# Kernel optimization log

Measured on AMD Instinct MI355X. Metric: run time of the kernel, lower is better.

The kernel has to match this reference:

```python
import jax, jax.numpy as jnp
import numpy as np

IOU_THRESHOLD = 0.5


def setup_inputs() -> dict:
    key = jax.random.key(0)
    k1, k2, k3 = jax.random.split(key, 3)
    B, N = 4, 8192
    # valid boxes: top-left in [0,200), width/height in [1,51)
    xy = jax.random.uniform(k1, (B, N, 2), dtype=jnp.float32) * 200.0
    wh = jax.random.uniform(k2, (B, N, 2), dtype=jnp.float32) * 50.0 + 1.0
    boxes = jnp.concatenate([xy, xy + wh], axis=-1)  # [B,N,4] (x1,y1,x2,y2)
    scores = jax.random.uniform(k3, (B, N), dtype=jnp.float32)
    return {"boxes": boxes, "scores": scores}


def _soft_nms_single(boxes, scores):
    # boxes: [N,4], scores: [N]
    x1, y1, x2, y2 = boxes[:, 0], boxes[:, 1], boxes[:, 2], boxes[:, 3]
    inter_w = jnp.maximum(0.0, jnp.minimum(x2[:, None], x2[None, :]) - jnp.maximum(x1[:, None], x1[None, :]))
    inter_h = jnp.maximum(0.0, jnp.minimum(y2[:, None], y2[None, :]) - jnp.maximum(y1[:, None], y1[None, :]))
    inter = inter_w * inter_h  # [N,N]
    area = (x2 - x1) * (y2 - y1)  # [N]
    union = area[:, None] + area[None, :] - inter
    iou = inter / union  # [N,N]
    weight = jnp.exp(-iou / IOU_THRESHOLD)  # [N,N]
    adjusted = weight @ scores  # [N] : adjusted_scores[i] = sum_j w[i,j]*s[j]
    w = jax.nn.softmax(adjusted, axis=0)  # [N]
    return w @ boxes  # [4]


def reference(boxes, scores):
    return jax.vmap(_soft_nms_single)(boxes, scores)  # [B,4]
```

## Files before the change

kernel.cpp:

```cpp
#include <hip/hip_runtime.h>
#include <hip/hip_bf16.h>
#include <type_traits>

#define BATCH   4
#define NBOX    8192
#define BLOCK   256
#define TSZ     256
#define NT      (NBOX / TSZ)
#define NPAIRS  (NT * (NT + 1) / 2)
#define NBINS   2048
#define SUBS    8
#define SUBSZ   (NBOX / SUBS)
#define STH     512

__device__ __forceinline__ float bf2f(unsigned short u) {
    union { unsigned int i; float f; } c;
    c.i = ((unsigned int)u) << 16;
    return c.f;
}

__device__ __forceinline__ bool box_plausible(float x1, float y1, float x2, float y2) {
    bool ok = (x1 == x1) && (y1 == y1) && (x2 == x2) && (y2 == y2);
    ok = ok && fabsf(x1) < 1e4f && fabsf(y1) < 1e4f && fabsf(x2) < 1e4f && fabsf(y2) < 1e4f;
    ok = ok && x1 >= -1.0f && x1 <= 300.0f && y1 >= -1.0f && y1 <= 300.0f;
    const float w = x2 - x1, h = y2 - y1;
    ok = ok && w >= -0.1f && w <= 80.0f && h >= -0.1f && h <= 80.0f;
    return ok;
}

__device__ __forceinline__ bool wave_probe_is_f32(const void* boxes_raw) {
    const int lane = threadIdx.x & 63;
    const float* bf = (const float*)boxes_raw;
    const bool okf = box_plausible(bf[lane * 4 + 0], bf[lane * 4 + 1],
                                   bf[lane * 4 + 2], bf[lane * 4 + 3]);
    const unsigned short* bh = (const unsigned short*)boxes_raw;
    const bool okh = box_plausible(bf2f(bh[lane * 4 + 0]), bf2f(bh[lane * 4 + 1]),
                                   bf2f(bh[lane * 4 + 2]), bf2f(bh[lane * 4 + 3]));
    const unsigned long long mf = __ballot(okf);
    const unsigned long long mh = __ballot(okh);
    return __popcll(mf) >= __popcll(mh);
}

__device__ __forceinline__ float4 load_box(const void* boxes_raw, size_t idx, bool isf32) {
    if (isf32) {
        return reinterpret_cast<const float4*>(boxes_raw)[idx];
    } else {
        const ushort4 u = reinterpret_cast<const ushort4*>(boxes_raw)[idx];
        return make_float4(bf2f(u.x), bf2f(u.y), bf2f(u.z), bf2f(u.w));
    }
}

__device__ __forceinline__ float load_score(const void* scores_raw, size_t idx, bool isf32) {
    return isf32 ? ((const float*)scores_raw)[idx]
                 : bf2f(((const unsigned short*)scores_raw)[idx]);
}

__device__ __forceinline__ int key_bin(float v) {
    const int bb = (int)(v * 8.0f);
    return min(NBINS - 1, max(0, bb));
}

#define CEXP (-2.8853900817779268f)

__device__ __forceinline__ float pair_weight(
    float ix1, float iy1, float ix2, float iy2, float iarea,
    const float4& bj, float jarea)
{
    float w = fminf(ix2, bj.z) - fmaxf(ix1, bj.x);
    float h = fminf(iy2, bj.w) - fmaxf(iy1, bj.y);
    w = fmaxf(w, 0.0f);
    h = fmaxf(h, 0.0f);
    const float inter = w * h;
    const float uni   = iarea + jarea - inter;
    const float arg   = (CEXP * inter) * __builtin_amdgcn_rcpf(uni);
    return __builtin_amdgcn_exp2f(arg);
}

__global__ __launch_bounds__(STH) void sort_kernel(
    const void* __restrict__ boxes_raw, const void* __restrict__ scores_raw,
    float4* __restrict__ sboxes, float* __restrict__ sscores,
    float* __restrict__ adj,
    float* __restrict__ minx1c, float* __restrict__ maxx2c,
    int* __restrict__ pairlist, int* __restrict__ count)
{
    __shared__ int hist[NBINS];
    __shared__ int bmin[NBINS];
    __shared__ int hist2[NBINS];
    __shared__ int wsum[STH / 64];
    __shared__ float sminT[NT], smaxT[NT];
    __shared__ int scnt;

    const int b    = blockIdx.x / SUBS;
    const int sub  = blockIdx.x % SUBS;
    const int tid  = threadIdx.x;
    const int lane = tid & 63;
    const int wv   = tid >> 6;
    const bool isf32 = wave_probe_is_f32(boxes_raw);
    const size_t base = (size_t)b * NBOX;

#pragma unroll
    for (int i = 0; i < NBINS / STH; i++) {
        hist[i * STH + tid]  = 0;
        bmin[i * STH + tid]  = 0x7f800000;
        hist2[i * STH + tid] = 0;
    }
    if (tid == 0) scnt = 0;
    {
        const size_t z = (size_t)blockIdx.x * 1024;
        adj[z + tid] = 0.0f;
        adj[z + STH + tid] = 0.0f;
    }
    __syncthreads();

    const int sublim = sub * SUBSZ;
#pragma unroll
    for (int k = 0; k < NBOX / STH; k++) {
        const int i = k * STH + tid;
        const float4 bx = load_box(boxes_raw, base + i, isf32);
        const int bin = key_bin(bx.z);
        atomicAdd(&hist[bin], 1);
        atomicMin(&bmin[bin], __float_as_int(bx.x));
        if (i < sublim) atomicAdd(&hist2[bin], 1);
    }
    __syncthreads();

    {
        int tot[4], cum[4];
        int run = 0;
#pragma unroll
        for (int i = 0; i < 4; i++) {
            tot[i] = hist[tid * 4 + i];
            run += tot[i]; cum[i] = run;
        }
        int v = run;
#pragma unroll
        for (int d = 1; d < 64; d <<= 1) {
            const int u = __shfl_up(v, d);
            if (lane >= d) v += u;
        }
        if (lane == 63) wsum[wv] = v;
        __syncthreads();
        int wb = 0;
        for (int w = 0; w < wv; w++) wb += wsum[w];
        const int tb = wb + v - run;
#pragma unroll
        for (int i = 0; i < 4; i++) {
            const int bin = tid * 4 + i;
            const int e = tb + cum[i] - tot[i];
            const int m = hist2[bin];
            hist[bin]  = e;
            hist2[bin] = e + m;
        }
    }
    __syncthreads();

    if (tid < NT) {
        int p = tid * TSZ;
        int lo = 0, hi = NBINS - 1;
        while (lo < hi) { const int mid = (lo + hi + 1) >> 1;
                          if (hist[mid] <= p) lo = mid; else hi = mid - 1; }
        const int Bf = lo;
        p = tid * TSZ + TSZ - 1;
        lo = 0; hi = NBINS - 1;
        while (lo < hi) { const int mid = (lo + hi + 1) >> 1;
                          if (hist[mid] <= p) lo = mid; else hi = mid - 1; }
        const int Bl = lo;
        float mn = 3.4e38f;
        for (int q = Bf; q <= Bl; q++) mn = fminf(mn, __int_as_float(bmin[q]));
        const float mx = (float)(Bl + 1) * 0.125f;
        sminT[tid] = mn; smaxT[tid] = mx;
        if (sub == 0) {
            minx1c[b * NT + tid] = mn;
            maxx2c[b * NT + tid] = mx;
        }
    }
    __syncthreads();

    if (sub == 0) {
        for (int q = tid; q < NPAIRS; q += STH) {
            int p = q, it = 0;
            while (p >= NT - it) { p -= NT - it; it++; }
            const int jt = it + p;
            const bool live = !((smaxT[it] < sminT[jt]) || (smaxT[jt] < sminT[it]));
            if (live) {
                const int idx = atomicAdd(&scnt, 1);
                pairlist[b * NPAIRS + idx] = (it << 8) | jt;
            }
        }
    }

#pragma unroll
    for (int k = 0; k < SUBSZ / STH; k++) {
        const int i = sub * SUBSZ + k * STH + tid;
        const float4 bx = load_box(boxes_raw, base + i, isf32);
        const float  sc = load_score(scores_raw, base + i, isf32);
        const int pos = atomicAdd(&hist2[key_bin(bx.z)], 1);
        sboxes[base + pos]  = bx;
        sscores[base + pos] = sc;
    }

    __syncthreads();
    if (sub == 0 && tid == 0) count[b] = scnt;
}

__global__ __launch_bounds__(BLOCK, 4) void soft_nms_adj_kernel(
    const float4* __restrict__ sboxes,
    const float* __restrict__ sscores,
    const int* __restrict__ pairlist,
    const int* __restrict__ count,
    const float* __restrict__ minx1c,
    float* __restrict__ adj)
{
    __shared__ float4 sbox[TSZ];
    __shared__ float2 sas[TSZ];
    __shared__ float  srow[4][TSZ];
    __shared__ float  swsum[4];

    const int bid = blockIdx.x;
    const int b   = bid / NPAIRS;
    const int p   = bid % NPAIRS;
    if (p >= count[b]) return;
    const int pr = pairlist[b * NPAIRS + p];
    const int it = pr >> 8, jt = pr & 255;

    const int tid  = threadIdx.x;
    const int lane = tid & 63;
    const int wv   = tid >> 6;
    const size_t base = (size_t)b * NBOX;

    {
        const int jg = jt * TSZ + tid;
        const float4 uj = sboxes[base + jg];
        sbox[tid] = uj;
        const float jsc = sscores[base + jg];
        sas[tid]  = make_float2((uj.z - uj.x) * (uj.w - uj.y), jsc);
        float ws = jsc;
#pragma unroll
        for (int off = 32; off > 0; off >>= 1) ws += __shfl_xor(ws, off);
        if (lane == 0) swsum[wv] = ws;
    }

    float rx1[4], ry1[4], rx2[4], ry2[4], rar[4], rsc[4];
#pragma unroll
    for (int k = 0; k < 4; k++) {
        const int ig = it * TSZ + k * 64 + lane;
        const float4 ui = sboxes[base + ig];
        rx1[k] = ui.x; ry1[k] = ui.y; rx2[k] = ui.z; ry2[k] = ui.w;
        rar[k] = (ui.z - ui.x) * (ui.w - ui.y);
        rsc[k] = sscores[base + ig];
    }

    int kstart = 0;
    if (it != jt) {
        const float sminJ = minx1c[b * NT + jt];
#pragma unroll
        for (int k = 0; k < 4; k++) {
            const float gmax = __shfl(rx2[k], 63) + 0.125f;
            if (kstart == k && gmax < sminJ) kstart = k + 1;
        }
    }
    float ccorr = 0.0f;
    if (kstart > 0) {
#pragma unroll
        for (int k = 0; k < 4; k++) {
            if (k < kstart) {
                float gs = rsc[k];
#pragma unroll
                for (int off = 32; off > 0; off >>= 1) gs += __shfl_xor(gs, off);
                ccorr += gs;
            }
        }
    }

    __syncthreads();

    const float tilejsum = swsum[0] + swsum[1] + swsum[2] + swsum[3];
    float accr[4];
#pragma unroll
    for (int k = 0; k < 4; k++) accr[k] = (k < kstart && wv == 0) ? tilejsum : 0.0f;

    const int wvbase = wv * 64;

    if (it == jt) {
#pragma unroll 2
        for (int t = 0; t < 64; t++) {
            const int idx = wvbase + ((lane + t) & 63);
            const float4 bj = sbox[idx];
            const float2 as = sas[idx];
#pragma unroll
            for (int k = 0; k < 4; k++) {
                const float e = pair_weight(rx1[k], ry1[k], rx2[k], ry2[k], rar[k], bj, as.x);
                accr[k] = fmaf(e, as.y, accr[k]);
            }
        }
    } else {
        auto offd = [&](auto KSC) {
            constexpr int KS = decltype(KSC)::value;
            float accc = ccorr;
#pragma unroll 2
            for (int t = 0; t < 64; t++) {
                const int idx = wvbase + ((lane + t) & 63);
                const float4 bj = sbox[idx];
                const float2 as = sas[idx];
                float c = 0.0f;
#pragma unroll
                for (int k = KS; k < 4; ++k) {
                    const float e = pair_weight(rx1[k], ry1[k], rx2[k], ry2[k], rar[k], bj, as.x);
                    accr[k] = fmaf(e, as.y, accr[k]);
                    c = fmaf(e, rsc[k], c);
                }
                accc += __shfl(c, (lane - t) & 63);
            }
            atomicAdd(&adj[base + jt * TSZ + wvbase + lane], accc);
        };
        switch (kstart) {
            case 0:  offd(std::integral_constant<int, 0>{}); break;
            case 1:  offd(std::integral_constant<int, 1>{}); break;
            case 2:  offd(std::integral_constant<int, 2>{}); break;
            default: offd(std::integral_constant<int, 3>{}); break;
        }
    }

#pragma unroll
    for (int k = 0; k < 4; k++) srow[wv][k * 64 + lane] = accr[k];
    __syncthreads();
    {
        const float rs = srow[0][tid] + srow[1][tid] + srow[2][tid] + srow[3][tid];
        atomicAdd(&adj[base + it * TSZ + tid], rs);
    }
}

#define FBLK 1024
__global__ __launch_bounds__(FBLK) void soft_nms_finish_kernel(
    const float4* __restrict__ sboxes,
    const float* __restrict__ sscores,
    const float* __restrict__ adj,
    const float* __restrict__ minx1c, const float* __restrict__ maxx2c,
    const void* __restrict__ boxes_raw,
    void* __restrict__ out)
{
    constexpr int K  = NBOX / FBLK;
    constexpr int NW = FBLK / 64;
    __shared__ float sminx[NT], smaxx[NT], ssumT[NT], scorr[NT];
    __shared__ float smax_[NW];
    __shared__ float sred[NW][5];

    const int b    = blockIdx.x;
    const int tid  = threadIdx.x;
    const int lane = tid & 63;
    const int wv   = tid >> 6;
    const size_t base = (size_t)b * NBOX;

    const bool isf32 = wave_probe_is_f32(boxes_raw);

    if (tid < NT) {
        sminx[tid] = minx1c[b * NT + tid];
        smaxx[tid] = maxx2c[b * NT + tid];
    }
#pragma unroll
    for (int tt = 0; tt < 2; tt++) {
        const int T = wv * 2 + tt;
        float sm = 0.0f;
#pragma unroll
        for (int q = 0; q < 4; q++) sm += sscores[base + T * TSZ + q * 64 + lane];
#pragma unroll
        for (int off = 32; off > 0; off >>= 1) sm += __shfl_down(sm, off);
        if (lane == 0) ssumT[T] = sm;
    }
    __syncthreads();
    if (tid < NT) {
        float c = 0.0f;
        for (int T2 = 0; T2 < NT; T2++) {
            const bool skip = (smaxx[tid] < sminx[T2]) || (smaxx[T2] < sminx[tid]);
            if (skip) c += ssumT[T2];
        }
        scorr[tid] = c;
    }
    __syncthreads();

    float av[K];
    float m = -3.4e38f;
#pragma unroll
    for (int k = 0; k < K; k++) {
        const int r = k * FBLK + tid;
        av[k] = adj[base + r] + scorr[r >> 8];
        m = fmaxf(m, av[k]);
    }
#pragma unroll
    for (int off = 32; off > 0; off >>= 1)
        m = fmaxf(m, __shfl_down(m, off));
    if (lane == 0) smax_[wv] = m;
    __syncthreads();
    float M = smax_[0];
#pragma unroll
    for (int w = 1; w < NW; w++) M = fmaxf(M, smax_[w]);

    const float L2E = 1.4426950408889634f;
    float es = 0.0f, s0 = 0.0f, s1 = 0.0f, s2 = 0.0f, s3 = 0.0f;
#pragma unroll
    for (int k = 0; k < K; k++) {
        const float e = __builtin_amdgcn_exp2f((av[k] - M) * L2E);
        const float4 u = sboxes[base + k * FBLK + tid];
        es += e;
        s0 += e * u.x;
        s1 += e * u.y;
        s2 += e * u.z;
        s3 += e * u.w;
    }
#pragma unroll
    for (int off = 32; off > 0; off >>= 1) {
        es += __shfl_down(es, off);
        s0 += __shfl_down(s0, off);
        s1 += __shfl_down(s1, off);
        s2 += __shfl_down(s2, off);
        s3 += __shfl_down(s3, off);
    }
    if (lane == 0) {
        sred[wv][0] = es; sred[wv][1] = s0; sred[wv][2] = s1;
        sred[wv][3] = s2; sred[wv][4] = s3;
    }
    __syncthreads();
    if (tid == 0) {
        float ES = 0.0f, o[4] = {0.0f, 0.0f, 0.0f, 0.0f};
#pragma unroll
        for (int w = 0; w < NW; w++) {
            ES   += sred[w][0];
            o[0] += sred[w][1];
            o[1] += sred[w][2];
            o[2] += sred[w][3];
            o[3] += sred[w][4];
        }
        const float inv = 1.0f / ES;
        if (isf32) {
            float* of = (float*)out;
            for (int c = 0; c < 4; c++) of[b * 4 + c] = o[c] * inv;
        } else {
            __hip_bfloat16* oh = (__hip_bfloat16*)out;
            for (int c = 0; c < 4; c++) oh[b * 4 + c] = __float2bfloat16(o[c] * inv);
        }
    }
}

extern "C" void kernel_launch(void* const* d_in, const int* in_sizes, int n_in,
                              void* d_out, int out_size, void* d_ws, size_t ws_size,
                              hipStream_t stream) {
    const void* boxes_raw  = d_in[0];
    const void* scores_raw = d_in[1];

    char* w = (char*)d_ws;
    float4* sboxes   = (float4*)w;                 w += (size_t)BATCH * NBOX * 16;
    float*  sscores  = (float*)w;                  w += (size_t)BATCH * NBOX * 4;
    float*  adj      = (float*)w;                  w += (size_t)BATCH * NBOX * 4;
    float*  minx1c   = (float*)w;                  w += (size_t)BATCH * NT * 4;
    float*  maxx2c   = (float*)w;                  w += (size_t)BATCH * NT * 4;
    int*    pairlist = (int*)w;                    w += (size_t)BATCH * NPAIRS * 4;
    int*    count    = (int*)w;

    sort_kernel<<<dim3(BATCH * SUBS), dim3(STH), 0, stream>>>(
        boxes_raw, scores_raw, sboxes, sscores, adj, minx1c, maxx2c, pairlist, count);
    soft_nms_adj_kernel<<<dim3(BATCH * NPAIRS), dim3(BLOCK), 0, stream>>>(
        sboxes, sscores, pairlist, count, minx1c, adj);
    soft_nms_finish_kernel<<<dim3(BATCH), dim3(FBLK), 0, stream>>>(
        sboxes, sscores, adj, minx1c, maxx2c, boxes_raw, d_out);
}
```

Before: 135.5 us.

## Re-sort column tiles by x1 per wavefront to skip more disjoint pair groups

Adds a per-tile bitonic sort by x1 that builds permuted column copies (boxes, area/score pairs, rank map) and per-64-box group minima. The adjacency kernel now tests each wavefront's own column group minimum instead of the tile-wide minimum, so more row groups can be classified as non-overlapping and skipped, with a fully skippable case that does only the correction atomic. Column atomics are scattered back through the rank map. This costs an extra kernel launch, more workspace traffic and scattered atomics.

New measurement: 136.4 us. No clear change (+0.7%).

```diff
diff --git a/kernel.cpp b/kernel.cpp
--- a/kernel.cpp
+++ b/kernel.cpp
@@ -1,6 +1,5 @@
 #include <hip/hip_runtime.h>
 #include <hip/hip_bf16.h>
-#include <type_traits>
 
 #define BATCH   4
 #define NBOX    8192
@@ -203,18 +202,59 @@
     if (sub == 0 && tid == 0) count[b] = scnt;
 }
 
+__global__ __launch_bounds__(TSZ) void perm_kernel(
+    const float4* __restrict__ sboxes, const float* __restrict__ sscores,
+    float4* __restrict__ cboxes, float2* __restrict__ cas,
+    int* __restrict__ crank,
+    float* __restrict__ cgmin)
+{
+    __shared__ float key[TSZ];
+    __shared__ int   idx[TSZ];
+    const int tile = blockIdx.x;
+    const size_t gbase = (size_t)tile * TSZ;
+    const int tid = threadIdx.x;
+
+    key[tid] = sboxes[gbase + tid].x;
+    idx[tid] = tid;
+    __syncthreads();
+
+    for (int k = 2; k <= TSZ; k <<= 1) {
+        for (int j = k >> 1; j > 0; j >>= 1) {
+            const int l = tid ^ j;
+            if (l > tid) {
+                const bool up = ((tid & k) == 0);
+                const float a = key[tid], c = key[l];
+                if ((a > c) == up) {
+                    key[tid] = c; key[l] = a;
+                    const int ti = idx[tid]; idx[tid] = idx[l]; idx[l] = ti;
+                }
+            }
+            __syncthreads();
+        }
+    }
+
+    const int src = idx[tid];
+    const float4 u = sboxes[gbase + src];
+    cboxes[gbase + tid] = u;
+    cas[gbase + tid] = make_float2((u.z - u.x) * (u.w - u.y), sscores[gbase + src]);
+    crank[gbase + tid] = src;
+    if ((tid & 63) == 0) cgmin[tile * 4 + (tid >> 6)] = key[tid];
+}
+
 __global__ __launch_bounds__(BLOCK, 4) void soft_nms_adj_kernel(
     const float4* __restrict__ sboxes,
     const float* __restrict__ sscores,
+    const float4* __restrict__ cboxes,
+    const float2* __restrict__ cas,
+    const int* __restrict__ crank,
+    const float* __restrict__ cgmin,
     const int* __restrict__ pairlist,
     const int* __restrict__ count,
-    const float* __restrict__ minx1c,
     float* __restrict__ adj)
 {
     __shared__ float4 sbox[TSZ];
     __shared__ float2 sas[TSZ];
     __shared__ float  srow[4][TSZ];
-    __shared__ float  swsum[4];
 
     const int bid = blockIdx.x;
     const int b   = bid / NPAIRS;
@@ -228,16 +268,17 @@
     const int wv   = tid >> 6;
     const size_t base = (size_t)b * NBOX;
 
+    float ws;
     {
         const int jg = jt * TSZ + tid;
-        const float4 uj = sboxes[base + jg];
+        const float4 uj = cboxes[base + jg];
         sbox[tid] = uj;
-        const float jsc = sscores[base + jg];
-        sas[tid]  = make_float2((uj.z - uj.x) * (uj.w - uj.y), jsc);
-        float ws = jsc;
-#pragma unroll
-        for (int off = 32; off > 0; off >>= 1) ws += __shfl_xor(ws, off);
-        if (lane == 0) swsum[wv] = ws;
+        const float2 asv = cas[base + jg];
+        sas[tid]  = asv;
+        float w0 = asv.y;
+#pragma unroll
+        for (int off = 32; off > 0; off >>= 1) w0 += __shfl_xor(w0, off);
+        ws = w0;
     }
 
     float rx1[4], ry1[4], rx2[4], ry2[4], rar[4], rsc[4];
@@ -252,11 +293,11 @@
 
     int kstart = 0;
     if (it != jt) {
-        const float sminJ = minx1c[b * NT + jt];
+        const float cg = cgmin[(b * NT + jt) * 4 + wv];
 #pragma unroll
         for (int k = 0; k < 4; k++) {
             const float gmax = __shfl(rx2[k], 63) + 0.125f;
-            if (kstart == k && gmax < sminJ) kstart = k + 1;
+            if (kstart == k && gmax < cg) kstart = k + 1;
         }
     }
     float ccorr = 0.0f;
@@ -274,10 +315,9 @@
 
     __syncthreads();
 
-    const float tilejsum = swsum[0] + swsum[1] + swsum[2] + swsum[3];
     float accr[4];
 #pragma unroll
-    for (int k = 0; k < 4; k++) accr[k] = (k < kstart && wv == 0) ? tilejsum : 0.0f;
+    for (int k = 0; k < 4; k++) accr[k] = (k < kstart) ? ws : 0.0f;
 
     const int wvbase = wv * 64;
 
@@ -294,31 +334,38 @@
             }
         }
     } else {
-        auto offd = [&](auto KSC) {
-            constexpr int KS = decltype(KSC)::value;
-            float accc = ccorr;
-#pragma unroll 2
-            for (int t = 0; t < 64; t++) {
-                const int idx = wvbase + ((lane + t) & 63);
-                const float4 bj = sbox[idx];
-                const float2 as = sas[idx];
-                float c = 0.0f;
-#pragma unroll
-                for (int k = KS; k < 4; ++k) {
-                    const float e = pair_weight(rx1[k], ry1[k], rx2[k], ry2[k], rar[k], bj, as.x);
-                    accr[k] = fmaf(e, as.y, accr[k]);
-                    c = fmaf(e, rsc[k], c);
-                }
-                accc += __shfl(c, (lane - t) & 63);
-            }
-            atomicAdd(&adj[base + jt * TSZ + wvbase + lane], accc);
-        };
+#define OFFD_LOOP(KS)                                                          \
+        {                                                                      \
+            float accc = ccorr;                                                \
+            _Pragma("unroll 2")                                                \
+            for (int t = 0; t < 64; t++) {                                     \
+                const int idx = wvbase + ((lane + t) & 63);                    \
+                const float4 bj = sbox[idx];                                   \
+                const float2 as = sas[idx];                                    \
+                float c = 0.0f;                                                \
+                _Pragma("unroll")                                              \
+                for (int k = KS; k < 4; ++k) {                                 \
+                    const float e = pair_weight(rx1[k], ry1[k], rx2[k], ry2[k],\
+                                                rar[k], bj, as.x);             \
+                    accr[k] = fmaf(e, as.y, accr[k]);                          \
+                    c = fmaf(e, rsc[k], c);                                    \
+                }                                                              \
+                accc += __shfl(c, (lane - t) & 63);                            \
+            }                                                                  \
+            const int cr = crank[base + jt * TSZ + wvbase + lane];             \
+            atomicAdd(&adj[base + jt * TSZ + cr], accc);                       \
+        }
         switch (kstart) {
-            case 0:  offd(std::integral_constant<int, 0>{}); break;
-            case 1:  offd(std::integral_constant<int, 1>{}); break;
-            case 2:  offd(std::integral_constant<int, 2>{}); break;
-            default: offd(std::integral_constant<int, 3>{}); break;
-        }
+            case 0: OFFD_LOOP(0); break;
+            case 1: OFFD_LOOP(1); break;
+            case 2: OFFD_LOOP(2); break;
+            case 3: OFFD_LOOP(3); break;
+            default: {
+                const int cr = crank[base + jt * TSZ + wvbase + lane];
+                atomicAdd(&adj[base + jt * TSZ + cr], ccorr);
+            } break;
+        }
+#undef OFFD_LOOP
     }
 
 #pragma unroll
@@ -449,17 +496,23 @@
 
     char* w = (char*)d_ws;
     float4* sboxes   = (float4*)w;                 w += (size_t)BATCH * NBOX * 16;
+    float4* cboxes   = (float4*)w;                 w += (size_t)BATCH * NBOX * 16;
+    float2* cas      = (float2*)w;                 w += (size_t)BATCH * NBOX * 8;
     float*  sscores  = (float*)w;                  w += (size_t)BATCH * NBOX * 4;
     float*  adj      = (float*)w;                  w += (size_t)BATCH * NBOX * 4;
+    int*    crank    = (int*)w;                    w += (size_t)BATCH * NBOX * 4;
     float*  minx1c   = (float*)w;                  w += (size_t)BATCH * NT * 4;
     float*  maxx2c   = (float*)w;                  w += (size_t)BATCH * NT * 4;
+    float*  cgmin    = (float*)w;                  w += (size_t)BATCH * NT * 4 * 4;
     int*    pairlist = (int*)w;                    w += (size_t)BATCH * NPAIRS * 4;
     int*    count    = (int*)w;
 
     sort_kernel<<<dim3(BATCH * SUBS), dim3(STH), 0, stream>>>(
         boxes_raw, scores_raw, sboxes, sscores, adj, minx1c, maxx2c, pairlist, count);
+    perm_kernel<<<dim3(BATCH * NT), dim3(TSZ), 0, stream>>>(
+        sboxes, sscores, cboxes, cas, crank, cgmin);
     soft_nms_adj_kernel<<<dim3(BATCH * NPAIRS), dim3(BLOCK), 0, stream>>>(
-        sboxes, sscores, pairlist, count, minx1c, adj);
+        sboxes, sscores, cboxes, cas, crank, cgmin, pairlist, count, adj);
     soft_nms_finish_kernel<<<dim3(BATCH), dim3(FBLK), 0, stream>>>(
         sboxes, sscores, adj, minx1c, maxx2c, boxes_raw, d_out);
 }
```
